# Kernel tuning notes

Measured on AMD Instinct MI355X. Metric: run time of the kernel, lower is better.

## Reference

```python
import jax, jax.numpy as jnp
import numpy as np

B, N, H, D, L = 2, 256, 256, 64, 6  # batch, pocket atoms, hidden dim, atom feat dim, EGNN layers


def _lin(x, w, b):
    return x @ w + b


def setup_inputs() -> dict:
    key = jax.random.key(0)
    ks = iter(jax.random.split(key, 64))

    def w(shape, s=0.05):
        return jax.random.normal(next(ks), shape, jnp.float32) * s

    inp = {
        'pocket_coords': jax.random.normal(next(ks), (B, N, 3), jnp.float32),
        'pocket_features': jax.random.normal(next(ks), (B, N, D), jnp.float32),
        't': jax.random.uniform(next(ks), (B,), jnp.float32, 0.0, 1000.0),
        'pe_w1': w((3 + D, H)), 'pe_b1': w((H,)),
        'pe_w2': w((H, H)), 'pe_b2': w((H,)),
        'pe_w3': w((H, H)), 'pe_b3': w((H,)),
        'te_w1': w((1, H)), 'te_b1': w((H,)),
        'te_w2': w((H, H)), 'te_b2': w((H,)),
        'ln_g': jnp.ones((L, H), jnp.float32), 'ln_b': jnp.zeros((L, H), jnp.float32),
        'ew1': w((L, 2 * H + 1, H)), 'eb1': w((L, H)),
        'ew2': w((L, H, H)), 'eb2': w((L, H)),
        'cw1': w((L, H, H)), 'cb1': w((L, H)),
        'cw2': w((L, H, 1)), 'cb2': w((L, 1)),
        'nw1': w((L, 2 * H, H)), 'nb1': w((L, H)),
        'nw2': w((L, H, H)), 'nb2': w((L, H)),
        'dec_w1': w((H, H)), 'dec_b1': w((H,)),
        'dec_w2': w((H, H)), 'dec_b2': w((H,)),
        'dec_w3': w((H, 3)), 'dec_b3': w((3,)),
    }
    return inp


def reference(pocket_coords, pocket_features, t,
              pe_w1, pe_b1, pe_w2, pe_b2, pe_w3, pe_b3,
              te_w1, te_b1, te_w2, te_b2,
              ln_g, ln_b,
              ew1, eb1, ew2, eb2,
              cw1, cb1, cw2, cb2,
              nw1, nb1, nw2, nb2,
              dec_w1, dec_b1, dec_w2, dec_b2, dec_w3, dec_b3):
    relu, silu = jax.nn.relu, jax.nn.silu

    # --- pocket encoder (residual MLP; in_dim 67 != H so no skip; dropout = identity at eval)
    pin = jnp.concatenate([pocket_coords, pocket_features], axis=-1)  # [B,N,3+D]
    h = relu(_lin(pin, pe_w1, pe_b1))
    h = relu(_lin(h, pe_w2, pe_b2))
    h = relu(_lin(h, pe_w3, pe_b3))

    # --- time embedding, broadcast over atoms
    te = relu(_lin(t[:, None], te_w1, te_b1))
    te = _lin(te, te_w2, te_b2)  # [B,H]
    h = h + te[:, None, :]

    # --- 6-layer dense EGNN (all-pairs), norm_feats=True -> LayerNorm on h per layer
    x = pocket_coords
    for l in range(L):
        h_in = h
        mu = h.mean(-1, keepdims=True)
        hc = h - mu
        hn = hc / jnp.sqrt((hc * hc).mean(-1, keepdims=True) + 1e-5) * ln_g[l] + ln_b[l]
        rel = x[:, :, None, :] - x[:, None, :, :]            # [B,N,N,3]
        d2 = jnp.sum(rel * rel, axis=-1, keepdims=True)      # [B,N,N,1]
        hi = jnp.broadcast_to(hn[:, :, None, :], (B, N, N, H))
        hj = jnp.broadcast_to(hn[:, None, :, :], (B, N, N, H))
        eij = jnp.concatenate([hi, hj, d2], axis=-1)         # [B,N,N,2H+1]
        m = silu(_lin(eij, ew1[l], eb1[l]))
        m = silu(_lin(m, ew2[l], eb2[l]))                    # [B,N,N,H] messages
        cw = _lin(silu(_lin(m, cw1[l], cb1[l])), cw2[l], cb2[l])  # [B,N,N,1]
        x = x + jnp.mean(rel * cw, axis=2)                   # equivariant coord update
        magg = jnp.sum(m, axis=2)                            # [B,N,H] aggregated messages
        u = silu(_lin(jnp.concatenate([hn, magg], axis=-1), nw1[l], nb1[l]))
        h = h_in + _lin(u, nw2[l], nb2[l])                   # residual node update

    # --- decoder (residual MLP, dims equal so skip applies before final projection)
    o = relu(_lin(h, dec_w1, dec_b1))
    o = relu(_lin(o, dec_w2, dec_b2)) + h
    return _lin(o, dec_w3, dec_b3)                           # predicted noise [B,N,3]
```

## Files before the change

kernel.cpp:

```cpp
#include <hip/hip_runtime.h>
#include <math.h>

static constexpr int NB = 2, NN = 256, HH = 256, DD = 64, LL = 6;
static constexpr int RN = NB * NN * HH;
static constexpr int SROWB = 528;

typedef __attribute__((ext_vector_type(8))) short bf16x8;
typedef __attribute__((ext_vector_type(4))) float f32x4;
typedef __attribute__((ext_vector_type(4))) float float4v;
typedef __attribute__((ext_vector_type(4))) unsigned int u32x4;

__device__ __forceinline__ float fsilu(float v) {
    return v * __builtin_amdgcn_rcpf(1.0f + __expf(-v));
}
__device__ __forceinline__ unsigned short f2bf(float f) {
    union { float f; unsigned int u; } x; x.f = f;
    unsigned int r = x.u + 0x7fffu + ((x.u >> 16) & 1u);
    return (unsigned short)(r >> 16);
}
__device__ __forceinline__ float bitsf(unsigned int u) {
    union { float f; unsigned int u; } x; x.u = u; return x.f;
}
__device__ __forceinline__ float bflo(unsigned int w) { return bitsf(w << 16); }
__device__ __forceinline__ float bfhi(unsigned int w) { return bitsf(w & 0xffff0000u); }
__device__ __forceinline__ unsigned int cvtpk(float lo, float hi) {
    unsigned int w;
    asm("v_cvt_pk_bf16_f32 %0, %1, %2" : "=v"(w) : "v"(lo), "v"(hi));
    return w;
}

__global__ void k_convert(const float* __restrict__ ew2, const float* __restrict__ cw1,
                          unsigned short* __restrict__ ew2P, unsigned short* __restrict__ cw1P) {
    int g = blockIdx.x * blockDim.x + threadIdx.x;
    if (g >= LL * 8192) return;
    int l = g >> 13;
    int r = g & 8191;
    int lane = r & 63;
    int fidx = r >> 6;
    int ks = fidx >> 4;
    int wv = (fidx >> 1) & 7;
    int ct = fidx & 1;
    int col = wv * 32 + ct * 16 + (lane & 15);
    int k0 = ks * 32 + (lane >> 4) * 8;
    #pragma unroll
    for (int e = 0; e < 8; ++e) {
        ew2P[(size_t)g * 8 + e] = f2bf(ew2[((size_t)l * HH + k0 + e) * HH + col]);
        cw1P[(size_t)g * 8 + e] = f2bf(cw1[((size_t)l * HH + k0 + e) * HH + col]);
    }
}

__global__ void k_convert2(const float* __restrict__ nw1, const float* __restrict__ nw2,
                           const float* __restrict__ ew1,
                           unsigned short* __restrict__ nw1B, unsigned short* __restrict__ nw2B,
                           unsigned short* __restrict__ ew1B) {
    int idx = blockIdx.x * blockDim.x + threadIdx.x;
    if (idx >= LL * 131072) return;
    int l = idx >> 17;
    int r = idx & 131071;
    int c = r >> 8, col = r & 255;
    int dst = (l << 17) + ((c >> 1) << 9) + (col << 1) + (c & 1);
    nw1B[dst] = f2bf(nw1[(size_t)l * 131072 + c * 256 + col]);
    ew1B[dst] = f2bf(ew1[(size_t)l * 131328 + c * 256 + col]);
    if (r < 65536) {
        int d2 = (l << 16) + ((c >> 1) << 9) + (col << 1) + (c & 1);
        nw2B[d2] = f2bf(nw2[(size_t)l * 65536 + c * 256 + col]);
    }
}

__global__ __launch_bounds__(256) void k_encoder(
    const float* __restrict__ coords, const float* __restrict__ feats, const float* __restrict__ t,
    const float* __restrict__ pw1, const float* __restrict__ pb1,
    const float* __restrict__ pw2, const float* __restrict__ pb2,
    const float* __restrict__ pw3, const float* __restrict__ pb3,
    const float* __restrict__ tw1, const float* __restrict__ tb1,
    const float* __restrict__ tw2, const float* __restrict__ tb2,
    float* __restrict__ h, float* __restrict__ x) {
    __shared__ float spinT[68][2];
    __shared__ float shaT[HH][2];
    __shared__ float shbT[HH][2];
    __shared__ float ste1[HH];
    int tid = threadIdx.x;
    int base = blockIdx.x * 2;
    int b = base / NN;

    #pragma unroll
    for (int r = 0; r < 2; ++r) {
        int row = base + r;
        if (tid < 3) spinT[tid][r] = coords[row * 3 + tid];
        if (tid < DD) spinT[3 + tid][r] = feats[row * DD + tid];
    }
    float tv = t[b];
    ste1[tid] = fmaxf(tv * tw1[tid] + tb1[tid], 0.0f);
    if (tid < 6) {
        int r = tid / 3, c = tid % 3;
        x[(base + r) * 3 + c] = coords[(base + r) * 3 + c];
    }
    __syncthreads();

    float a0 = pb1[tid], a1 = a0;
    for (int c = 0; c < 67; ++c) {
        float w = pw1[c * HH + tid];
        float2 s = *(const float2*)&spinT[c][0];
        a0 += s.x * w; a1 += s.y * w;
    }
    shaT[tid][0] = fmaxf(a0, 0.f); shaT[tid][1] = fmaxf(a1, 0.f);
    __syncthreads();
    a0 = pb2[tid]; a1 = a0;
    for (int c = 0; c < HH; ++c) {
        float w = pw2[c * HH + tid];
        float2 s = *(const float2*)&shaT[c][0];
        a0 += s.x * w; a1 += s.y * w;
    }
    shbT[tid][0] = fmaxf(a0, 0.f); shbT[tid][1] = fmaxf(a1, 0.f);
    __syncthreads();
    a0 = pb3[tid]; a1 = a0;
    float te = tb2[tid];
    for (int c = 0; c < HH; ++c) {
        float w = pw3[c * HH + tid];
        float2 s = *(const float2*)&shbT[c][0];
        a0 += s.x * w; a1 += s.y * w;
        te += ste1[c] * tw2[c * HH + tid];
    }
    h[(base + 0) * HH + tid] = fmaxf(a0, 0.f) + te;
    h[(base + 1) * HH + tid] = fmaxf(a1, 0.f) + te;
}

__global__ __launch_bounds__(256) void k_ln_aiaj(
    const float* __restrict__ h, const float* __restrict__ g, const float* __restrict__ bta,
    const unsigned int* __restrict__ ew1w, const float* __restrict__ eb1l,
    float* __restrict__ hn, float* __restrict__ Ai, unsigned short* __restrict__ AjB) {
    __shared__ float shnT[HH][2];
    int tid = threadIdx.x, wv = tid >> 6, lane = tid & 63;
    int base = blockIdx.x * 2;

    if (wv < 2) {
        int row = base + wv;
        float v[4];
        #pragma unroll
        for (int q = 0; q < 4; ++q) v[q] = h[row * HH + lane + 64 * q];
        float s = v[0] + v[1] + v[2] + v[3];
        #pragma unroll
        for (int m = 1; m < 64; m <<= 1) s += __shfl_xor(s, m);
        float mu = s * (1.0f / HH);
        float var = 0.f;
        #pragma unroll
        for (int q = 0; q < 4; ++q) { v[q] -= mu; var += v[q] * v[q]; }
        #pragma unroll
        for (int m = 1; m < 64; m <<= 1) var += __shfl_xor(var, m);
        float rstd = rsqrtf(var * (1.0f / HH) + 1e-5f);
        #pragma unroll
        for (int q = 0; q < 4; ++q) {
            int k = lane + 64 * q;
            float hv = v[q] * rstd * g[k] + bta[k];
            shnT[k][wv] = hv;
            hn[row * HH + k] = hv;
        }
    }
    __syncthreads();

    float ai0 = eb1l[tid], ai1 = ai0;
    float aj0 = 0.f, aj1 = 0.f;
    for (int c2 = 0; c2 < 128; ++c2) {
        unsigned int wip = ew1w[c2 * 256 + tid];
        unsigned int wjp = ew1w[(128 + c2) * 256 + tid];
        float4 s = *(const float4*)&shnT[c2 * 2][0];
        ai0 += s.x * bflo(wip) + s.z * bfhi(wip);
        ai1 += s.y * bflo(wip) + s.w * bfhi(wip);
        aj0 += s.x * bflo(wjp) + s.z * bfhi(wjp);
        aj1 += s.y * bflo(wjp) + s.w * bfhi(wjp);
    }
    Ai[(base + 0) * HH + tid] = ai0; AjB[(base + 0) * HH + tid] = f2bf(aj0);
    Ai[(base + 1) * HH + tid] = ai1; AjB[(base + 1) * HH + tid] = f2bf(aj1);
}

__global__ __launch_bounds__(512, 1) void k_edge(
    const float* __restrict__ x, const float* __restrict__ Ai, const unsigned short* __restrict__ AjB,
    const float* __restrict__ wd, const float* __restrict__ eb2v,
    const unsigned short* __restrict__ ew2P, const unsigned short* __restrict__ cw1P,
    const float* __restrict__ cb1v, const float* __restrict__ cw2v, const float* __restrict__ cb2p,
    float* __restrict__ magg, float* __restrict__ xdelta) {
    __shared__ float srel[128][3];
    __shared__ float sd2[128];
    __shared__ float cwpart[8][128];
    __shared__ char s_tile[128 * SROWB];
    __shared__ char m_tile[128 * SROWB];

    int tid = threadIdx.x, wv = tid >> 6, lane = tid & 63;
    int g4 = lane >> 4, l15 = lane & 15;
    int colbase = wv * 32;
    int bi = blockIdx.x;
    int b = bi >> 8, i = bi & 255;
    int ni = b * NN + i;
    int bbase = b * NN;
    int bthr = ((wv << 7) + lane) << 3;

    int k0p = (tid & 31) << 3;
    float aiv[8], wdv[8];
    {
        float4v a0 = *(const float4v*)(Ai + (size_t)ni * HH + k0p);
        float4v a1 = *(const float4v*)(Ai + (size_t)ni * HH + k0p + 4);
        float4v w0 = *(const float4v*)(wd + k0p);
        float4v w1 = *(const float4v*)(wd + k0p + 4);
        #pragma unroll
        for (int e = 0; e < 4; ++e) { aiv[e] = a0[e]; aiv[4 + e] = a1[e]; wdv[e] = w0[e]; wdv[4 + e] = w1[e]; }
    }
    float eb2r[2], cb1r[2], cw2r[2];
    #pragma unroll
    for (int ct = 0; ct < 2; ++ct) {
        int col = colbase + ct * 16 + l15;
        eb2r[ct] = eb2v[col]; cb1r[ct] = cb1v[col]; cw2r[ct] = cw2v[col];
    }
    float xi0 = x[ni * 3 + 0], xi1 = x[ni * 3 + 1], xi2 = x[ni * 3 + 2];
    float cb2 = cb2p[0];

    bf16x8 Bew[8][2], Bcw[8][2];
    #pragma unroll
    for (int ks = 0; ks < 8; ++ks) {
        #pragma unroll
        for (int ct = 0; ct < 2; ++ct) {
            Bew[ks][ct] = *(const bf16x8*)(ew2P + (ks << 13) + (ct << 9) + bthr);
            Bcw[ks][ct] = *(const bf16x8*)(cw1P + (ks << 13) + (ct << 9) + bthr);
        }
    }

    char* p1w = s_tile + ((tid >> 5) * SROWB + k0p * 2);
    const char* aA = s_tile + (l15 * SROWB + g4 * 16);
    const char* aM = m_tile + (l15 * SROWB + g4 * 16);
    char* mwA = m_tile + ((g4 * 4) * SROWB + (colbase + l15) * 2);
    float mgv[2] = {0.f, 0.f};
    float xd0 = 0.f, xd1 = 0.f, xd2 = 0.f;

    #pragma unroll 1
    for (int jc = 0; jc < 2; ++jc) {
        int j0 = jc * 128;
        __syncthreads();
        if (tid < 128) {
            int j = bbase + j0 + tid;
            float rx = xi0 - x[j * 3 + 0];
            float ry = xi1 - x[j * 3 + 1];
            float rz = xi2 - x[j * 3 + 2];
            srel[tid][0] = rx; srel[tid][1] = ry; srel[tid][2] = rz;
            sd2[tid] = rx * rx + ry * ry + rz * rz;
        }
        __syncthreads();

        #pragma unroll
        for (int it = 0; it < 8; ++it) {
            int row = it * 16 + (tid >> 5);
            float d2v = sd2[row];
            u32x4 ajw = *(const u32x4*)(AjB + ((size_t)(bbase + j0 + row) * HH + k0p));
            unsigned int uw0, uw1, uw2, uw3;
            uw0 = cvtpk(fsilu(aiv[0] + bflo(ajw[0]) + d2v * wdv[0]), fsilu(aiv[1] + bfhi(ajw[0]) + d2v * wdv[1]));
            uw1 = cvtpk(fsilu(aiv[2] + bflo(ajw[1]) + d2v * wdv[2]), fsilu(aiv[3] + bfhi(ajw[1]) + d2v * wdv[3]));
            uw2 = cvtpk(fsilu(aiv[4] + bflo(ajw[2]) + d2v * wdv[4]), fsilu(aiv[5] + bfhi(ajw[2]) + d2v * wdv[5]));
            uw3 = cvtpk(fsilu(aiv[6] + bflo(ajw[3]) + d2v * wdv[6]), fsilu(aiv[7] + bfhi(ajw[3]) + d2v * wdv[7]));
            u32x4 sv = {uw0, uw1, uw2, uw3};
            *reinterpret_cast<u32x4*>(p1w + it * 16 * SROWB) = sv;
        }
        __syncthreads();

        #pragma unroll 1
        for (int rh = 0; rh < 4; ++rh) {
            f32x4 acc[2][2];
            acc[0][0] = (f32x4){0.f,0.f,0.f,0.f}; acc[0][1] = (f32x4){0.f,0.f,0.f,0.f};
            acc[1][0] = (f32x4){0.f,0.f,0.f,0.f}; acc[1][1] = (f32x4){0.f,0.f,0.f,0.f};
            const char* aBase = aA + rh * 32 * SROWB;
            #pragma unroll
            for (int ks = 0; ks < 8; ++ks) {
                bf16x8 a0 = *reinterpret_cast<const bf16x8*>(aBase + ks * 64);
                bf16x8 a1 = *reinterpret_cast<const bf16x8*>(aBase + 16 * SROWB + ks * 64);
                acc[0][0] = __builtin_amdgcn_mfma_f32_16x16x32_bf16(a0, Bew[ks][0], acc[0][0], 0, 0, 0);
                acc[0][1] = __builtin_amdgcn_mfma_f32_16x16x32_bf16(a0, Bew[ks][1], acc[0][1], 0, 0, 0);
                acc[1][0] = __builtin_amdgcn_mfma_f32_16x16x32_bf16(a1, Bew[ks][0], acc[1][0], 0, 0, 0);
                acc[1][1] = __builtin_amdgcn_mfma_f32_16x16x32_bf16(a1, Bew[ks][1], acc[1][1], 0, 0, 0);
            }
            char* mw = mwA + rh * 32 * SROWB;
            #pragma unroll
            for (int rt = 0; rt < 2; ++rt) {
                #pragma unroll
                for (int r = 0; r < 4; ++r) {
                    float v0 = fsilu(acc[rt][0][r] + eb2r[0]);
                    float v1 = fsilu(acc[rt][1][r] + eb2r[1]);
                    mgv[0] += v0; mgv[1] += v1;
                    unsigned int w = cvtpk(v0, v1);
                    char* p = mw + (rt * 16 + r) * SROWB;
                    *reinterpret_cast<unsigned short*>(p) = (unsigned short)w;
                    *reinterpret_cast<unsigned short*>(p + 32) = (unsigned short)(w >> 16);
                }
            }
        }
        __syncthreads();

        #pragma unroll 1
        for (int rh = 0; rh < 4; ++rh) {
            f32x4 acc[2][2];
            acc[0][0] = (f32x4){0.f,0.f,0.f,0.f}; acc[0][1] = (f32x4){0.f,0.f,0.f,0.f};
            acc[1][0] = (f32x4){0.f,0.f,0.f,0.f}; acc[1][1] = (f32x4){0.f,0.f,0.f,0.f};
            const char* aBase = aM + rh * 32 * SROWB;
            #pragma unroll
            for (int ks = 0; ks < 8; ++ks) {
                bf16x8 a0 = *reinterpret_cast<const bf16x8*>(aBase + ks * 64);
                bf16x8 a1 = *reinterpret_cast<const bf16x8*>(aBase + 16 * SROWB + ks * 64);
                acc[0][0] = __builtin_amdgcn_mfma_f32_16x16x32_bf16(a0, Bcw[ks][0], acc[0][0], 0, 0, 0);
                acc[0][1] = __builtin_amdgcn_mfma_f32_16x16x32_bf16(a0, Bcw[ks][1], acc[0][1], 0, 0, 0);
                acc[1][0] = __builtin_amdgcn_mfma_f32_16x16x32_bf16(a1, Bcw[ks][0], acc[1][0], 0, 0, 0);
                acc[1][1] = __builtin_amdgcn_mfma_f32_16x16x32_bf16(a1, Bcw[ks][1], acc[1][1], 0, 0, 0);
            }
            float rs[8];
            #pragma unroll
            for (int q = 0; q < 8; ++q) rs[q] = 0.f;
            #pragma unroll
            for (int ct = 0; ct < 2; ++ct) {
                #pragma unroll
                for (int rt = 0; rt < 2; ++rt)
                    #pragma unroll
                    for (int r = 0; r < 4; ++r)
                        rs[rt * 4 + r] += fsilu(acc[rt][ct][r] + cb1r[ct]) * cw2r[ct];
            }
            #pragma unroll
            for (int m = 1; m <= 8; m <<= 1)
                #pragma unroll
                for (int q = 0; q < 8; ++q) rs[q] += __shfl_xor(rs[q], m);
            if (l15 == 0) {
                #pragma unroll
                for (int rt = 0; rt < 2; ++rt)
                    #pragma unroll
                    for (int r = 0; r < 4; ++r)
                        cwpart[wv][rh * 32 + rt * 16 + g4 * 4 + r] = rs[rt * 4 + r];
            }
        }
        __syncthreads();
        if (tid < 64) {
            #pragma unroll 1
            for (int q = 0; q < 2; ++q) {
                int lr = q * 64 + tid;
                float cwv = cb2;
                #pragma unroll
                for (int w = 0; w < 8; ++w) cwv += cwpart[w][lr];
                float p0 = srel[lr][0] * cwv;
                float p1 = srel[lr][1] * cwv;
                float p2 = srel[lr][2] * cwv;
                #pragma unroll
                for (int m = 1; m < 64; m <<= 1) {
                    p0 += __shfl_xor(p0, m); p1 += __shfl_xor(p1, m); p2 += __shfl_xor(p2, m);
                }
                xd0 += p0; xd1 += p1; xd2 += p2;
            }
        }
    }

    #pragma unroll
    for (int ct = 0; ct < 2; ++ct) {
        mgv[ct] += __shfl_xor(mgv[ct], 16);
        mgv[ct] += __shfl_xor(mgv[ct], 32);
    }
    if (lane < 16) {
        #pragma unroll
        for (int ct = 0; ct < 2; ++ct)
            magg[(size_t)ni * HH + colbase + ct * 16 + lane] = mgv[ct];
    }
    if (tid == 0) {
        xdelta[ni * 3 + 0] = xd0 * (1.0f / NN);
        xdelta[ni * 3 + 1] = xd1 * (1.0f / NN);
        xdelta[ni * 3 + 2] = xd2 * (1.0f / NN);
    }
}

__global__ __launch_bounds__(256) void k_node_ln(
    const float* __restrict__ hn, const float* __restrict__ magg,
    const unsigned int* __restrict__ nw1w, const float* __restrict__ nb1l,
    const unsigned int* __restrict__ nw2w, const float* __restrict__ nb2l,
    float* __restrict__ h, float* __restrict__ x, const float* __restrict__ xdelta,
    const float* __restrict__ g, const float* __restrict__ bta,
    const unsigned int* __restrict__ ew1w, const float* __restrict__ eb1l,
    float* __restrict__ hnout, float* __restrict__ Ai, unsigned short* __restrict__ AjB,
    int has_ln) {
    __shared__ float s2T[2 * HH][2];
    __shared__ float suT[HH][2];
    __shared__ float sh[2][HH];
    __shared__ float shnT[HH][2];
    int tid = threadIdx.x;
    int base = blockIdx.x * 2;
    #pragma unroll
    for (int r = 0; r < 2; ++r) {
        s2T[tid][r] = hn[(base + r) * HH + tid];
        s2T[HH + tid][r] = magg[(base + r) * HH + tid];
    }
    if (tid < 6) {
        int r = tid / 3, c = tid % 3;
        x[(base + r) * 3 + c] += xdelta[(base + r) * 3 + c];
    }
    __syncthreads();
    float a0 = nb1l[tid], a1 = a0;
    for (int c2 = 0; c2 < 256; ++c2) {
        unsigned int wp = nw1w[c2 * 256 + tid];
        float4 s = *(const float4*)&s2T[c2 * 2][0];
        a0 += s.x * bflo(wp) + s.z * bfhi(wp);
        a1 += s.y * bflo(wp) + s.w * bfhi(wp);
    }
    suT[tid][0] = fsilu(a0); suT[tid][1] = fsilu(a1);
    __syncthreads();
    float d0 = nb2l[tid], d1 = d0;
    for (int c2 = 0; c2 < 128; ++c2) {
        unsigned int wp = nw2w[c2 * 256 + tid];
        float4 s = *(const float4*)&suT[c2 * 2][0];
        d0 += s.x * bflo(wp) + s.z * bfhi(wp);
        d1 += s.y * bflo(wp) + s.w * bfhi(wp);
    }
    float h0 = h[(base + 0) * HH + tid] + d0;
    float h1 = h[(base + 1) * HH + tid] + d1;
    h[(base + 0) * HH + tid] = h0;
    h[(base + 1) * HH + tid] = h1;
    if (!has_ln) return;
    sh[0][tid] = h0; sh[1][tid] = h1;
    __syncthreads();

    int wv = tid >> 6, lane = tid & 63;
    if (wv < 2) {
        int row = base + wv;
        float v[4];
        #pragma unroll
        for (int q = 0; q < 4; ++q) v[q] = sh[wv][lane + 64 * q];
        float s = v[0] + v[1] + v[2] + v[3];
        #pragma unroll
        for (int m = 1; m < 64; m <<= 1) s += __shfl_xor(s, m);
        float mu = s * (1.0f / HH);
        float var = 0.f;
        #pragma unroll
        for (int q = 0; q < 4; ++q) { v[q] -= mu; var += v[q] * v[q]; }
        #pragma unroll
        for (int m = 1; m < 64; m <<= 1) var += __shfl_xor(var, m);
        float rstd = rsqrtf(var * (1.0f / HH) + 1e-5f);
        #pragma unroll
        for (int q = 0; q < 4; ++q) {
            int k = lane + 64 * q;
            float hv = v[q] * rstd * g[k] + bta[k];
            shnT[k][wv] = hv;
            hnout[row * HH + k] = hv;
        }
    }
    __syncthreads();

    float ai0 = eb1l[tid], ai1 = ai0;
    float aj0 = 0.f, aj1 = 0.f;
    for (int c2 = 0; c2 < 128; ++c2) {
        unsigned int wip = ew1w[c2 * 256 + tid];
        unsigned int wjp = ew1w[(128 + c2) * 256 + tid];
        float4 s = *(const float4*)&shnT[c2 * 2][0];
        ai0 += s.x * bflo(wip) + s.z * bfhi(wip);
        ai1 += s.y * bflo(wip) + s.w * bfhi(wip);
        aj0 += s.x * bflo(wjp) + s.z * bfhi(wjp);
        aj1 += s.y * bflo(wjp) + s.w * bfhi(wjp);
    }
    Ai[(base + 0) * HH + tid] = ai0; AjB[(base + 0) * HH + tid] = f2bf(aj0);
    Ai[(base + 1) * HH + tid] = ai1; AjB[(base + 1) * HH + tid] = f2bf(aj1);
}

__global__ __launch_bounds__(256) void k_decoder(
    const float* __restrict__ h,
    const float* __restrict__ dw1, const float* __restrict__ db1,
    const float* __restrict__ dw2, const float* __restrict__ db2,
    const float* __restrict__ dw3, const float* __restrict__ db3,
    float* __restrict__ out) {
    __shared__ float shT[HH][2];
    __shared__ float so1T[HH][2];
    __shared__ float so2T[HH][2];
    int tid = threadIdx.x;
    int base = blockIdx.x * 2;
    #pragma unroll
    for (int r = 0; r < 2; ++r) shT[tid][r] = h[(base + r) * HH + tid];
    __syncthreads();
    float a0 = db1[tid], a1 = a0;
    for (int c = 0; c < HH; ++c) {
        float w = dw1[c * HH + tid];
        float2 s = *(const float2*)&shT[c][0];
        a0 += s.x * w; a1 += s.y * w;
    }
    so1T[tid][0] = fmaxf(a0, 0.f); so1T[tid][1] = fmaxf(a1, 0.f);
    __syncthreads();
    a0 = db2[tid]; a1 = a0;
    for (int c = 0; c < HH; ++c) {
        float w = dw2[c * HH + tid];
        float2 s = *(const float2*)&so1T[c][0];
        a0 += s.x * w; a1 += s.y * w;
    }
    so2T[tid][0] = fmaxf(a0, 0.f) + shT[tid][0];
    so2T[tid][1] = fmaxf(a1, 0.f) + shT[tid][1];
    __syncthreads();
    if (tid < 6) {
        int r = tid / 3, c = tid % 3;
        float acc = db3[c];
        for (int k = 0; k < HH; ++k) acc += so2T[k][r] * dw3[k * 3 + c];
        out[(base + r) * 3 + c] = acc;
    }
}

extern "C" void kernel_launch(void* const* d_in, const int* in_sizes, int n_in,
                              void* d_out, int out_size, void* d_ws, size_t ws_size,
                              hipStream_t stream) {
    const float* coords = (const float*)d_in[0];
    const float* feats  = (const float*)d_in[1];
    const float* t      = (const float*)d_in[2];
    const float* pe_w1  = (const float*)d_in[3];  const float* pe_b1 = (const float*)d_in[4];
    const float* pe_w2  = (const float*)d_in[5];  const float* pe_b2 = (const float*)d_in[6];
    const float* pe_w3  = (const float*)d_in[7];  const float* pe_b3 = (const float*)d_in[8];
    const float* te_w1  = (const float*)d_in[9];  const float* te_b1 = (const float*)d_in[10];
    const float* te_w2  = (const float*)d_in[11]; const float* te_b2 = (const float*)d_in[12];
    const float* ln_g   = (const float*)d_in[13]; const float* ln_b  = (const float*)d_in[14];
    const float* ew1    = (const float*)d_in[15]; const float* eb1   = (const float*)d_in[16];
    const float* ew2    = (const float*)d_in[17]; const float* eb2   = (const float*)d_in[18];
    const float* cw1    = (const float*)d_in[19]; const float* cb1   = (const float*)d_in[20];
    const float* cw2    = (const float*)d_in[21]; const float* cb2   = (const float*)d_in[22];
    const float* nw1    = (const float*)d_in[23]; const float* nb1   = (const float*)d_in[24];
    const float* nw2    = (const float*)d_in[25]; const float* nb2   = (const float*)d_in[26];
    const float* dec_w1 = (const float*)d_in[27]; const float* dec_b1 = (const float*)d_in[28];
    const float* dec_w2 = (const float*)d_in[29]; const float* dec_b2 = (const float*)d_in[30];
    const float* dec_w3 = (const float*)d_in[31]; const float* dec_b3 = (const float*)d_in[32];

    float* ws = (float*)d_ws;
    float* h      = ws;
    float* hn     = ws + RN;
    float* Ai     = ws + 2 * RN;
    float* magg   = ws + 3 * RN;
    float* x      = ws + 4 * RN;
    float* xdelta = ws + 4 * RN + 2048;
    unsigned short* AjB  = (unsigned short*)(ws + 4 * RN + 4096);
    unsigned short* ew2P = AjB + RN;
    unsigned short* cw1P = ew2P + LL * HH * HH;
    unsigned short* nw1B = cw1P + LL * HH * HH;
    unsigned short* ew1B = nw1B + LL * 2 * HH * HH;
    unsigned short* nw2B = ew1B + LL * 2 * HH * HH;

    k_convert<<<(LL * 8192 + 511) / 512, 512, 0, stream>>>(ew2, cw1, ew2P, cw1P);
    k_convert2<<<(LL * 131072 + 255) / 256, 256, 0, stream>>>(nw1, nw2, ew1, nw1B, nw2B, ew1B);
    k_encoder<<<NB * NN / 2, 256, 0, stream>>>(coords, feats, t,
        pe_w1, pe_b1, pe_w2, pe_b2, pe_w3, pe_b3, te_w1, te_b1, te_w2, te_b2, h, x);
    k_ln_aiaj<<<NB * NN / 2, 256, 0, stream>>>(h, ln_g, ln_b,
        (const unsigned int*)ew1B, eb1, hn, Ai, AjB);

    for (int l = 0; l < LL; ++l) {
        k_edge<<<NB * NN, 512, 0, stream>>>(x, Ai, AjB,
            ew1 + ((size_t)l * 513 + 512) * HH, eb2 + l * HH,
            ew2P + (size_t)l * HH * HH, cw1P + (size_t)l * HH * HH,
            cb1 + l * HH, cw2 + l * HH, cb2 + l, magg, xdelta);
        int ln = (l + 1 < LL) ? (l + 1) : LL - 1;
        k_node_ln<<<NB * NN / 2, 256, 0, stream>>>(hn, magg,
            (const unsigned int*)(nw1B + (size_t)l * 2 * HH * HH), nb1 + l * HH,
            (const unsigned int*)(nw2B + (size_t)l * HH * HH), nb2 + l * HH, h, x, xdelta,
            ln_g + ln * HH, ln_b + ln * HH,
            (const unsigned int*)(ew1B + (size_t)ln * 2 * HH * HH), eb1 + ln * HH,
            hn, Ai, AjB, (l + 1 < LL) ? 1 : 0);
    }

    k_decoder<<<NB * NN / 2, 256, 0, stream>>>(h, dec_w1, dec_b1, dec_w2, dec_b2,
                                               dec_w3, dec_b3, (float*)d_out);
}
```

Before: 627.5 us.

## Fuse node update, LayerNorm and next-layer Ai/Aj projection into edge kernel

Removes the separate k_node_ln launch. Each edge block now finishes its own row: node MLP, residual, LayerNorm, and the next layer's Ai/Aj projection, with the K dimension split across 512 threads. To avoid races with other blocks still reading this layer's inputs, x, Ai and Aj are ping-ponged between two buffers. This saves a launch and the magg/xdelta round trip per layer, but each block now processes one row instead of two, so it reads the node weights twice as often and adds serial tail work to the edge kernel.

```diff
diff --git a/kernel.cpp b/kernel.cpp
--- a/kernel.cpp
+++ b/kernel.cpp
@@ -178,10 +178,17 @@
     const float* __restrict__ wd, const float* __restrict__ eb2v,
     const unsigned short* __restrict__ ew2P, const unsigned short* __restrict__ cw1P,
     const float* __restrict__ cb1v, const float* __restrict__ cw2v, const float* __restrict__ cb2p,
-    float* __restrict__ magg, float* __restrict__ xdelta) {
+    float* __restrict__ h, float* __restrict__ hn,
+    float* __restrict__ xnext, float* __restrict__ Ainext, unsigned short* __restrict__ AjBnext,
+    const unsigned int* __restrict__ nw1w, const float* __restrict__ nb1l,
+    const unsigned int* __restrict__ nw2w, const float* __restrict__ nb2l,
+    const float* __restrict__ gamv, const float* __restrict__ betv,
+    const unsigned int* __restrict__ ew1wn, const float* __restrict__ eb1n,
+    int has_ln) {
     __shared__ float srel[128][3];
     __shared__ float sd2[128];
     __shared__ float cwpart[8][128];
+    __shared__ float smagg[256];
     __shared__ char s_tile[128 * SROWB];
     __shared__ char m_tile[128 * SROWB];
 
@@ -355,105 +362,95 @@
         mgv[ct] += __shfl_xor(mgv[ct], 32);
     }
     if (lane < 16) {
-        #pragma unroll
-        for (int ct = 0; ct < 2; ++ct)
-            magg[(size_t)ni * HH + colbase + ct * 16 + lane] = mgv[ct];
-    }
-    if (tid == 0) {
-        xdelta[ni * 3 + 0] = xd0 * (1.0f / NN);
-        xdelta[ni * 3 + 1] = xd1 * (1.0f / NN);
-        xdelta[ni * 3 + 2] = xd2 * (1.0f / NN);
-    }
-}
-
-__global__ __launch_bounds__(256) void k_node_ln(
-    const float* __restrict__ hn, const float* __restrict__ magg,
-    const unsigned int* __restrict__ nw1w, const float* __restrict__ nb1l,
-    const unsigned int* __restrict__ nw2w, const float* __restrict__ nb2l,
-    float* __restrict__ h, float* __restrict__ x, const float* __restrict__ xdelta,
-    const float* __restrict__ g, const float* __restrict__ bta,
-    const unsigned int* __restrict__ ew1w, const float* __restrict__ eb1l,
-    float* __restrict__ hnout, float* __restrict__ Ai, unsigned short* __restrict__ AjB,
-    int has_ln) {
-    __shared__ float s2T[2 * HH][2];
-    __shared__ float suT[HH][2];
-    __shared__ float sh[2][HH];
-    __shared__ float shnT[HH][2];
-    int tid = threadIdx.x;
-    int base = blockIdx.x * 2;
-    #pragma unroll
-    for (int r = 0; r < 2; ++r) {
-        s2T[tid][r] = hn[(base + r) * HH + tid];
-        s2T[HH + tid][r] = magg[(base + r) * HH + tid];
-    }
-    if (tid < 6) {
-        int r = tid / 3, c = tid % 3;
-        x[(base + r) * 3 + c] += xdelta[(base + r) * 3 + c];
-    }
-    __syncthreads();
-    float a0 = nb1l[tid], a1 = a0;
-    for (int c2 = 0; c2 < 256; ++c2) {
-        unsigned int wp = nw1w[c2 * 256 + tid];
-        float4 s = *(const float4*)&s2T[c2 * 2][0];
-        a0 += s.x * bflo(wp) + s.z * bfhi(wp);
-        a1 += s.y * bflo(wp) + s.w * bfhi(wp);
-    }
-    suT[tid][0] = fsilu(a0); suT[tid][1] = fsilu(a1);
-    __syncthreads();
-    float d0 = nb2l[tid], d1 = d0;
-    for (int c2 = 0; c2 < 128; ++c2) {
-        unsigned int wp = nw2w[c2 * 256 + tid];
-        float4 s = *(const float4*)&suT[c2 * 2][0];
-        d0 += s.x * bflo(wp) + s.z * bfhi(wp);
-        d1 += s.y * bflo(wp) + s.w * bfhi(wp);
-    }
-    float h0 = h[(base + 0) * HH + tid] + d0;
-    float h1 = h[(base + 1) * HH + tid] + d1;
-    h[(base + 0) * HH + tid] = h0;
-    h[(base + 1) * HH + tid] = h1;
+        smagg[colbase + lane] = mgv[0];
+        smagg[colbase + 16 + lane] = mgv[1];
+    }
+    if (has_ln && tid == 0) {
+        xnext[ni * 3 + 0] = xi0 + xd0 * (1.0f / NN);
+        xnext[ni * 3 + 1] = xi1 + xd1 * (1.0f / NN);
+        xnext[ni * 3 + 2] = xi2 + xd2 * (1.0f / NN);
+    }
+    __syncthreads();
+
+    float* s2v   = (float*)s_tile;
+    float* part  = (float*)(s_tile + 4096);
+    float* suv   = (float*)(s_tile + 8192);
+    float* shrow = (float*)(s_tile + 12288);
+    float* shnv  = (float*)(s_tile + 16384);
+    float* red   = (float*)(s_tile + 20480);
+
+    if (tid < 256) {
+        s2v[tid] = hn[(size_t)ni * HH + tid];
+        s2v[HH + tid] = smagg[tid];
+    }
+    __syncthreads();
+    {
+        int col = tid & 255, kh = tid >> 8;
+        const unsigned int* w = nw1w + (kh * 128) * 256;
+        const float* sv = s2v + kh * 256;
+        float p = 0.f;
+        for (int c2 = 0; c2 < 128; ++c2) {
+            unsigned int wp = w[c2 * 256 + col];
+            float2 sp = *(const float2*)&sv[c2 * 2];
+            p += sp.x * bflo(wp) + sp.y * bfhi(wp);
+        }
+        part[tid] = p;
+    }
+    __syncthreads();
+    if (tid < 256) suv[tid] = fsilu(part[tid] + part[256 + tid] + nb1l[tid]);
+    __syncthreads();
+    {
+        int col = tid & 255, kh = tid >> 8;
+        const unsigned int* w = nw2w + (kh * 64) * 256;
+        const float* sv = suv + kh * 128;
+        float p = 0.f;
+        for (int c2 = 0; c2 < 64; ++c2) {
+            unsigned int wp = w[c2 * 256 + col];
+            float2 sp = *(const float2*)&sv[c2 * 2];
+            p += sp.x * bflo(wp) + sp.y * bfhi(wp);
+        }
+        part[tid] = p;
+    }
+    __syncthreads();
+    if (tid < 256) {
+        float hv = h[(size_t)ni * HH + tid] + part[tid] + part[256 + tid] + nb2l[tid];
+        h[(size_t)ni * HH + tid] = hv;
+        shrow[tid] = hv;
+    }
+    __syncthreads();
     if (!has_ln) return;
-    sh[0][tid] = h0; sh[1][tid] = h1;
-    __syncthreads();
-
-    int wv = tid >> 6, lane = tid & 63;
-    if (wv < 2) {
-        int row = base + wv;
-        float v[4];
-        #pragma unroll
-        for (int q = 0; q < 4; ++q) v[q] = sh[wv][lane + 64 * q];
-        float s = v[0] + v[1] + v[2] + v[3];
-        #pragma unroll
-        for (int m = 1; m < 64; m <<= 1) s += __shfl_xor(s, m);
-        float mu = s * (1.0f / HH);
-        float var = 0.f;
-        #pragma unroll
-        for (int q = 0; q < 4; ++q) { v[q] -= mu; var += v[q] * v[q]; }
-        #pragma unroll
-        for (int m = 1; m < 64; m <<= 1) var += __shfl_xor(var, m);
-        float rstd = rsqrtf(var * (1.0f / HH) + 1e-5f);
-        #pragma unroll
-        for (int q = 0; q < 4; ++q) {
-            int k = lane + 64 * q;
-            float hv = v[q] * rstd * g[k] + bta[k];
-            shnT[k][wv] = hv;
-            hnout[row * HH + k] = hv;
-        }
-    }
-    __syncthreads();
-
-    float ai0 = eb1l[tid], ai1 = ai0;
-    float aj0 = 0.f, aj1 = 0.f;
-    for (int c2 = 0; c2 < 128; ++c2) {
-        unsigned int wip = ew1w[c2 * 256 + tid];
-        unsigned int wjp = ew1w[(128 + c2) * 256 + tid];
-        float4 s = *(const float4*)&shnT[c2 * 2][0];
-        ai0 += s.x * bflo(wip) + s.z * bfhi(wip);
-        ai1 += s.y * bflo(wip) + s.w * bfhi(wip);
-        aj0 += s.x * bflo(wjp) + s.z * bfhi(wjp);
-        aj1 += s.y * bflo(wjp) + s.w * bfhi(wjp);
-    }
-    Ai[(base + 0) * HH + tid] = ai0; AjB[(base + 0) * HH + tid] = f2bf(aj0);
-    Ai[(base + 1) * HH + tid] = ai1; AjB[(base + 1) * HH + tid] = f2bf(aj1);
+
+    {
+        float v = (tid < 256) ? shrow[tid] : 0.f;
+        float s1 = v, sq = v * v;
+        #pragma unroll
+        for (int m = 1; m < 64; m <<= 1) { s1 += __shfl_xor(s1, m); sq += __shfl_xor(sq, m); }
+        if (lane == 0) { red[wv] = s1; red[8 + wv] = sq; }
+    }
+    __syncthreads();
+    {
+        float mu  = (red[0] + red[1] + red[2] + red[3]) * (1.0f / HH);
+        float msq = (red[8] + red[9] + red[10] + red[11]) * (1.0f / HH);
+        float rstd = rsqrtf(msq - mu * mu + 1e-5f);
+        if (tid < 256) {
+            float hv = (shrow[tid] - mu) * rstd * gamv[tid] + betv[tid];
+            shnv[tid] = hv;
+            hn[(size_t)ni * HH + tid] = hv;
+        }
+    }
+    __syncthreads();
+    {
+        int col = tid & 255, hf = tid >> 8;
+        const unsigned int* w = ew1wn + (hf * 128) * 256;
+        float p = (hf == 0) ? eb1n[col] : 0.f;
+        for (int c2 = 0; c2 < 128; ++c2) {
+            unsigned int wp = w[c2 * 256 + col];
+            float2 sp = *(const float2*)&shnv[c2 * 2];
+            p += sp.x * bflo(wp) + sp.y * bfhi(wp);
+        }
+        if (hf == 0) Ainext[(size_t)ni * HH + col] = p;
+        else AjBnext[(size_t)ni * HH + col] = f2bf(p);
+    }
 }
 
 __global__ __launch_bounds__(256) void k_decoder(
@@ -518,14 +515,15 @@
     const float* dec_w3 = (const float*)d_in[31]; const float* dec_b3 = (const float*)d_in[32];
 
     float* ws = (float*)d_ws;
-    float* h      = ws;
-    float* hn     = ws + RN;
-    float* Ai     = ws + 2 * RN;
-    float* magg   = ws + 3 * RN;
-    float* x      = ws + 4 * RN;
-    float* xdelta = ws + 4 * RN + 2048;
-    unsigned short* AjB  = (unsigned short*)(ws + 4 * RN + 4096);
-    unsigned short* ew2P = AjB + RN;
+    float* h    = ws;
+    float* hn   = ws + RN;
+    float* Ai0  = ws + 2 * RN;
+    float* Ai1  = ws + 3 * RN;
+    float* xb0  = ws + 4 * RN;
+    float* xb1  = ws + 4 * RN + 2048;
+    unsigned short* Aj0  = (unsigned short*)(ws + 4 * RN + 4096);
+    unsigned short* Aj1  = Aj0 + RN;
+    unsigned short* ew2P = Aj1 + RN;
     unsigned short* cw1P = ew2P + LL * HH * HH;
     unsigned short* nw1B = cw1P + LL * HH * HH;
     unsigned short* ew1B = nw1B + LL * 2 * HH * HH;
@@ -534,22 +532,28 @@
     k_convert<<<(LL * 8192 + 511) / 512, 512, 0, stream>>>(ew2, cw1, ew2P, cw1P);
     k_convert2<<<(LL * 131072 + 255) / 256, 256, 0, stream>>>(nw1, nw2, ew1, nw1B, nw2B, ew1B);
     k_encoder<<<NB * NN / 2, 256, 0, stream>>>(coords, feats, t,
-        pe_w1, pe_b1, pe_w2, pe_b2, pe_w3, pe_b3, te_w1, te_b1, te_w2, te_b2, h, x);
+        pe_w1, pe_b1, pe_w2, pe_b2, pe_w3, pe_b3, te_w1, te_b1, te_w2, te_b2, h, xb0);
     k_ln_aiaj<<<NB * NN / 2, 256, 0, stream>>>(h, ln_g, ln_b,
-        (const unsigned int*)ew1B, eb1, hn, Ai, AjB);
+        (const unsigned int*)ew1B, eb1, hn, Ai0, Aj0);
 
     for (int l = 0; l < LL; ++l) {
-        k_edge<<<NB * NN, 512, 0, stream>>>(x, Ai, AjB,
+        const float* xin = (l & 1) ? xb1 : xb0;
+        float* xout      = (l & 1) ? xb0 : xb1;
+        const float* AiIn = (l & 1) ? Ai1 : Ai0;
+        float* AiOut      = (l & 1) ? Ai0 : Ai1;
+        const unsigned short* AjIn = (l & 1) ? Aj1 : Aj0;
+        unsigned short* AjOut      = (l & 1) ? Aj0 : Aj1;
+        int ln = (l + 1 < LL) ? (l + 1) : LL - 1;
+        k_edge<<<NB * NN, 512, 0, stream>>>(xin, AiIn, AjIn,
             ew1 + ((size_t)l * 513 + 512) * HH, eb2 + l * HH,
             ew2P + (size_t)l * HH * HH, cw1P + (size_t)l * HH * HH,
-            cb1 + l * HH, cw2 + l * HH, cb2 + l, magg, xdelta);
-        int ln = (l + 1 < LL) ? (l + 1) : LL - 1;
-        k_node_ln<<<NB * NN / 2, 256, 0, stream>>>(hn, magg,
+            cb1 + l * HH, cw2 + l * HH, cb2 + l,
+            h, hn, xout, AiOut, AjOut,
             (const unsigned int*)(nw1B + (size_t)l * 2 * HH * HH), nb1 + l * HH,
-            (const unsigned int*)(nw2B + (size_t)l * HH * HH), nb2 + l * HH, h, x, xdelta,
+            (const unsigned int*)(nw2B + (size_t)l * HH * HH), nb2 + l * HH,
             ln_g + ln * HH, ln_b + ln * HH,
             (const unsigned int*)(ew1B + (size_t)ln * 2 * HH * HH), eb1 + ln * HH,
-            hn, Ai, AjB, (l + 1 < LL) ? 1 : 0);
+            (l + 1 < LL) ? 1 : 0);
     }
 
     k_decoder<<<NB * NN / 2, 256, 0, stream>>>(h, dec_w1, dec_b1, dec_w2, dec_b2,
```

After: 580.9 us. 7.4% less time.
